# Kernel optimization log

Measured on AMD Instinct MI355X. Metric: run time of the kernel, lower is better.

## Reference

```python
import jax, jax.numpy as jnp
import numpy as np

FEAT_STRIDE = 16
PRE_NMS_TOP_N = 6000
POST_NMS_TOP_N = 300
NMS_THRESH = 0.7
A = 9  # len(scales)*len(ratios)
NEG = jnp.float32(-1e10)


def _generate_base_anchors(base_size=16, ratios=(0.5, 1.0, 2.0), scales=(8, 16, 32)):
    ratios = np.array(ratios, dtype=np.float64)
    scales = np.array(scales, dtype=np.float64)
    ctr = (base_size - 1) * 0.5
    size = float(base_size * base_size)
    ws = np.round(np.sqrt(size / ratios))
    hs = np.round(ws * ratios)
    out = []
    for w, h in zip(ws, hs):
        ws2 = w * scales
        hs2 = h * scales
        out.append(np.stack([ctr - 0.5 * (ws2 - 1), ctr - 0.5 * (hs2 - 1),
                             ctr + 0.5 * (ws2 - 1), ctr + 0.5 * (hs2 - 1)], axis=1))
    return np.concatenate(out, axis=0).astype(np.float32)  # [A,4]


def _all_anchors(H, W):
    base = _generate_base_anchors()
    sx = np.arange(W) * FEAT_STRIDE
    sy = np.arange(H) * FEAT_STRIDE
    sx, sy = np.meshgrid(sx, sy)  # [H,W] each, y-major ravel matches HW flatten
    shifts = np.stack([sx.ravel(), sy.ravel(), sx.ravel(), sy.ravel()], axis=1).astype(np.float32)
    return (shifts[:, None, :] + base[None, :, :]).reshape(-1, 4)  # [H*W*A,4]


def _nms_image(boxes, scores):
    # Greedy NMS on [N,4] boxes / [N] scores; emits top POST_NMS_TOP_N kept (padded with 0s).
    x1, y1, x2, y2 = boxes[:, 0], boxes[:, 1], boxes[:, 2], boxes[:, 3]
    areas = (x2 - x1 + 1.0) * (y2 - y1 + 1.0)

    def body(i, carry):
        live, ob, os_ = carry
        idx = jnp.argmax(live)
        s = live[idx]
        valid = s > NEG * 0.5
        b = boxes[idx]
        xx1 = jnp.maximum(b[0], x1)
        yy1 = jnp.maximum(b[1], y1)
        xx2 = jnp.minimum(b[2], x2)
        yy2 = jnp.minimum(b[3], y2)
        inter = jnp.maximum(xx2 - xx1 + 1.0, 0.0) * jnp.maximum(yy2 - yy1 + 1.0, 0.0)
        iou = inter / (areas[idx] + areas - inter)
        live = jnp.where(iou > NMS_THRESH, NEG, live)  # suppresses self too (iou=1)
        ob = ob.at[i].set(jnp.where(valid, b, 0.0))
        os_ = os_.at[i].set(jnp.where(valid, s, 0.0))
        return live, ob, os_

    init = (scores,
            jnp.zeros((POST_NMS_TOP_N, 4), boxes.dtype),
            jnp.zeros((POST_NMS_TOP_N,), scores.dtype))
    _, ob, os_ = jax.lax.fori_loop(0, POST_NMS_TOP_N, body, init)
    return ob, os_


def setup_inputs() -> dict:
    key = jax.random.key(0)
    ks = jax.random.split(key, 4)
    B, C, H, W = 4, 1024, 64, 64
    base_feat = jax.random.normal(ks[0], (B, C, H, W), jnp.float32)
    im_info = jnp.tile(jnp.array([H * 16.0, W * 16.0, 1.0], jnp.float32), (B, 1))
    gt_boxes = jnp.zeros((B, 20, 5), jnp.float32)   # unused in eval path
    num_boxes = jnp.zeros((B,), jnp.int32)           # unused in eval path
    conv_w = 0.01 * jax.random.normal(ks[1], (512, C, 3, 3), jnp.float32)
    conv_b = jnp.zeros((512,), jnp.float32)
    cls_w = 0.01 * jax.random.normal(ks[2], (2 * A, 512, 1, 1), jnp.float32)
    cls_b = jnp.zeros((2 * A,), jnp.float32)
    bbox_w = 0.01 * jax.random.normal(ks[3], (4 * A, 512, 1, 1), jnp.float32)
    bbox_b = jnp.zeros((4 * A,), jnp.float32)
    return {"base_feat": base_feat, "im_info": im_info, "gt_boxes": gt_boxes,
            "num_boxes": num_boxes, "conv_w": conv_w, "conv_b": conv_b,
            "cls_w": cls_w, "cls_b": cls_b, "bbox_w": bbox_w, "bbox_b": bbox_b}


def reference(base_feat, im_info, gt_boxes, num_boxes, conv_w, conv_b, cls_w, cls_b, bbox_w, bbox_b):
    B, _, H, W = base_feat.shape
    dn = ("NCHW", "OIHW", "NCHW")
    x = jax.lax.conv_general_dilated(base_feat, conv_w, (1, 1), [(1, 1), (1, 1)], dimension_numbers=dn)
    x = jax.nn.relu(x + conv_b[None, :, None, None])  # RPN_Conv + ReLU, [B,512,H,W]
    cls = jax.lax.conv_general_dilated(x, cls_w, (1, 1), "VALID", dimension_numbers=dn) + cls_b[None, :, None, None]
    bbox = jax.lax.conv_general_dilated(x, bbox_w, (1, 1), "VALID", dimension_numbers=dn) + bbox_b[None, :, None, None]

    # reshape(x,2) -> softmax over the 2-way axis: channel c pairs with c+A
    prob = jax.nn.softmax(cls.reshape(B, 2, A, H, W), axis=1)
    fg = prob[:, 1]                                   # [B,A,H,W] foreground probs
    scores = fg.transpose(0, 2, 3, 1).reshape(B, -1)  # [B, H*W*A]
    deltas = bbox.transpose(0, 2, 3, 1).reshape(B, -1, 4)

    anchors = jnp.asarray(_all_anchors(H, W))         # [H*W*A,4]
    wa = anchors[:, 2] - anchors[:, 0] + 1.0
    ha = anchors[:, 3] - anchors[:, 1] + 1.0
    cxa = anchors[:, 0] + 0.5 * (wa - 1.0)
    cya = anchors[:, 1] + 0.5 * (ha - 1.0)

    cx = deltas[..., 0] * wa + cxa
    cy = deltas[..., 1] * ha + cya
    pw = jnp.exp(deltas[..., 2]) * wa
    ph = jnp.exp(deltas[..., 3]) * ha
    x1 = cx - 0.5 * pw
    y1 = cy - 0.5 * ph
    x2 = cx + 0.5 * pw
    y2 = cy + 0.5 * ph

    imh = im_info[:, 0:1]
    imw = im_info[:, 1:2]
    x1 = jnp.clip(x1, 0.0, imw - 1.0)
    y1 = jnp.clip(y1, 0.0, imh - 1.0)
    x2 = jnp.clip(x2, 0.0, imw - 1.0)
    y2 = jnp.clip(y2, 0.0, imh - 1.0)
    boxes = jnp.stack([x1, y1, x2, y2], axis=-1)      # [B,N,4]

    s_top, idx = jax.lax.top_k(scores, PRE_NMS_TOP_N)
    b_top = jnp.take_along_axis(boxes, idx[:, :, None], axis=1)  # [B,6000,4]

    kept_boxes, kept_scores = jax.vmap(_nms_image)(b_top, s_top)  # [B,300,4],[B,300]
    bidx = jnp.broadcast_to(jnp.arange(B, dtype=kept_boxes.dtype).reshape(B, 1, 1),
                            (B, POST_NMS_TOP_N, 1))
    rois = jnp.concatenate([bidx, kept_boxes], axis=-1)  # [B,300,5]
    return rois, kept_scores
```

## Files before the change

kernel.cpp:

```cpp
#include <hip/hip_runtime.h>
#include <stdint.h>

#define HH_ 64
#define WW_ 64
#define NB 4
#define CIN 1024
#define CMID 512
#define NANCH (HH_*WW_*9)
#define PRE_N 6000
#define POST_N 300
#define CAND_PAD 6144
#define NEGV (-1.0e10f)
#define LO_SCL 2048.0f
#define LO_INV 4.8828125e-4f
#define MWORDS 192

typedef unsigned short u16;
typedef unsigned long long u64;
typedef __attribute__((ext_vector_type(8))) _Float16 f16x8;
typedef __attribute__((ext_vector_type(4))) float f32x4;

#define AS1 __attribute__((address_space(1)))
#define AS3 __attribute__((address_space(3)))

#define X_OFF   0
#define X_SZ    (NB*CMID*HH_*WW_)
#define SC_OFF  (X_OFF + X_SZ)
#define SC_SZ   (NB*NANCH)
#define BX_OFF  (SC_OFF + SC_SZ)
#define BX_SZ   (NB*NANCH*4)
#define CSC_OFF (BX_OFF + BX_SZ)
#define CSC_SZ  (NB*CAND_PAD)
#define CBX_OFF (CSC_OFF + CSC_SZ)
#define CBX_SZ  (NB*CAND_PAD*4)
#define CIX_OFF (CBX_OFF + CBX_SZ)
#define CIX_SZ  (NB*CAND_PAD)
#define WTH_OFF (CIX_OFF + CIX_SZ)
#define WTH_SZ  (9*512*1024/2)
#define WTL_OFF (WTH_OFF + WTH_SZ)
#define WTL_SZ  WTH_SZ
#define XH_OFF  (WTL_OFF + WTL_SZ)
#define XH_SZ   (NB*4096*1024/2)
#define XL_OFF  (XH_OFF + XH_SZ)
#define XL_SZ   XH_SZ
#define ZP_OFF  (XL_OFF + XL_SZ)
#define ZP_SZ   256

__device__ __forceinline__ void gl2lds16(const void* g, void* l) {
    __builtin_amdgcn_global_load_lds((const AS1 unsigned int*)g,
                                     (AS3 unsigned int*)l, 16, 0, 0);
}
union fh_u { _Float16 h; u16 u; };
__device__ __forceinline__ u16 f2h_hi(float x) {
    fh_u c; c.h = (_Float16)x; return c.u;
}
__device__ __forceinline__ u16 f2h_lo(float x, u16 hi) {
    fh_u c; c.u = hi;
    float hf = (float)c.h;
    fh_u d; d.h = (_Float16)((x - hf) * LO_SCL);
    return d.u;
}
__device__ __forceinline__ int cperm(int c) {
    int blk = c >> 5, w = c & 31;
    int pos = (w < 16) ? (((w >> 2) << 3) + (w & 3))
                       : ((((w - 16) >> 2) << 3) + 4 + (w & 3));
    return (blk << 5) + pos;
}
__device__ __forceinline__ unsigned fflip(unsigned u) {
    return (u & 0x80000000u) ? ~u : (u | 0x80000000u);
}

__global__ __launch_bounds__(256) void prep_wtk(
    const float* __restrict__ conv_w, u16* __restrict__ WTH,
    u16* __restrict__ WTL, float* __restrict__ ZP)
{
    int o = blockIdx.x * 256 + threadIdx.x;
    int ci = o & 1023, co = (o >> 10) & 511, r = o >> 19;
    float v = conv_w[((size_t)(co * 1024 + ci)) * 9 + r];
    u16 h  = f2h_hi(v);
    u16 lo = f2h_lo(v, h);
    size_t d = (((size_t)(r * 512 + co)) << 10) + cperm(ci);
    WTH[d] = h; WTL[d] = lo;
    if (o < 256) ZP[o] = 0.f;
}

__global__ __launch_bounds__(256) void prep_act(
    const float* __restrict__ in, u16* __restrict__ XH, u16* __restrict__ XL)
{
    __shared__ float T[64][65];
    const int blk = blockIdx.x;
    const int b   = blk >> 10;
    const int ci0 = ((blk >> 6) & 15) << 6;
    const int sp0 = (blk & 63) << 6;
    const int tid = threadIdx.x;
    const int tq  = tid >> 6;
    const int t64 = tid & 63;
#pragma unroll
    for (int w = 0; w < 16; w++) {
        int ci_l = w * 4 + tq;
        T[ci_l][t64] = in[(((size_t)(b * 1024 + ci0 + ci_l)) << 12) + sp0 + t64];
    }
    __syncthreads();
#pragma unroll
    for (int w = 0; w < 16; w++) {
        int sp_l = w * 4 + tq;
        float x = T[t64][sp_l];
        u16 h  = f2h_hi(x);
        u16 lo = f2h_lo(x, h);
        size_t d = (((size_t)((b << 12) + sp0 + sp_l)) << 10) + ci0 + cperm(t64);
        XH[d] = h; XL[d] = lo;
    }
}

__global__ __launch_bounds__(256, 2) void conv3_mfma(
    const u16* __restrict__ WTH, const u16* __restrict__ WTL,
    const u16* __restrict__ XH, const u16* __restrict__ XL,
    const u16* __restrict__ ZP, const float* __restrict__ bias,
    float* __restrict__ Xout)
{
    __shared__ u16 Ah_s[2][4096];
    __shared__ u16 Al_s[2][4096];
    __shared__ u16 Bh_s[2][4096];
    __shared__ u16 Bl_s[2][4096];

    const int tid = threadIdx.x;
    const int bn  = blockIdx.x;
    const int bm  = blockIdx.y;
    const int l   = tid & 63;
    const int wid = tid >> 6, wm = wid >> 1, wn = wid & 1;

    const int rowq = tid >> 2;
    const int c8   = (tid & 3) << 3;

    int spb[2]; unsigned vmq[2];
#pragma unroll
    for (int q = 0; q < 2; q++) {
        int n = bn * 128 + q * 64 + rowq;
        int yy = (n >> 6) & 63, xx = n & 63;
        spb[q] = n;
        unsigned m9 = 0;
#pragma unroll
        for (int rr = 0; rr < 9; rr++) {
            int dy = rr / 3 - 1, dx = rr % 3 - 1;
            if ((unsigned)(yy + dy) < 64u && (unsigned)(xx + dx) < 64u)
                m9 |= 1u << rr;
        }
        vmq[q] = m9;
    }

    f32x4 acc0[4][4], acc1[4][4];
#pragma unroll
    for (int i = 0; i < 4; i++)
#pragma unroll
        for (int j = 0; j < 4; j++) { acc0[i][j] = (f32x4)0.f; acc1[i][j] = (f32x4)0.f; }

    const int NK = 288;

    auto stage = [&](int sb, int kt) {
        const int r   = kt >> 5;
        const int ci0 = (kt & 31) << 5;
        const int kr  = (r * 11) >> 5;
        const int sh  = (kr - 1) * 64 + (r - 3 * kr - 1);
        const size_t wbase = (((size_t)(r * 512 + bm * 128)) << 10) + ci0 + c8;
        u16* ah = &Ah_s[sb][tid * 8];
        u16* al = &Al_s[sb][tid * 8];
        u16* bh = &Bh_s[sb][tid * 8];
        u16* bl = &Bl_s[sb][tid * 8];
#pragma unroll
        for (int q = 0; q < 2; q++) {
            const size_t aoff = wbase + (((size_t)(q * 64 + rowq)) << 10);
            gl2lds16(WTH + aoff, ah + q * 2048);
            gl2lds16(WTL + aoff, al + q * 2048);
            const bool v = (vmq[q] >> r) & 1u;
            const size_t boff = (((size_t)(spb[q] + sh)) << 10) + ci0 + c8;
            gl2lds16(v ? (XH + boff) : ZP, bh + q * 2048);
            gl2lds16(v ? (XL + boff) : ZP, bl + q * 2048);
        }
    };

    stage(0, 0);
    int buf = 0;
    for (int kt = 0; kt < NK; ++kt) {
        __syncthreads();
        if (kt + 1 < NK) stage(buf ^ 1, kt + 1);
        {
            const int lo16 = l & 15, hi4 = l >> 4;
            const int aoff = (wm * 64 + lo16) * 32 + hi4 * 8;
            const int boff = (wn * 64 + lo16) * 32 + hi4 * 8;
            f16x8 ah[4], av[4], bh[4], bv[4];
#pragma unroll
            for (int i = 0; i < 4; i++) {
                ah[i] = *(const f16x8*)&Ah_s[buf][aoff + i * 512];
                av[i] = *(const f16x8*)&Al_s[buf][aoff + i * 512];
                bh[i] = *(const f16x8*)&Bh_s[buf][boff + i * 512];
                bv[i] = *(const f16x8*)&Bl_s[buf][boff + i * 512];
            }
#pragma unroll
            for (int mi = 0; mi < 4; mi++)
#pragma unroll
                for (int ni = 0; ni < 4; ni++) {
                    acc0[mi][ni] = __builtin_amdgcn_mfma_f32_16x16x32_f16(
                        ah[mi], bh[ni], acc0[mi][ni], 0, 0, 0);
                    acc1[mi][ni] = __builtin_amdgcn_mfma_f32_16x16x32_f16(
                        ah[mi], bv[ni], acc1[mi][ni], 0, 0, 0);
                    acc1[mi][ni] = __builtin_amdgcn_mfma_f32_16x16x32_f16(
                        av[mi], bh[ni], acc1[mi][ni], 0, 0, 0);
                }
        }
        buf ^= 1;
    }

#pragma unroll
    for (int mi = 0; mi < 4; mi++) {
        const int co0 = bm * 128 + wm * 64 + mi * 16 + ((l >> 4) << 2);
        const f32x4 b4 = *(const f32x4*)&bias[co0];
#pragma unroll
        for (int ni = 0; ni < 4; ni++) {
            const int n = bn * 128 + wn * 64 + ni * 16 + (l & 15);
            const int b = n >> 12, sp = n & 4095;
            f32x4 v0 = acc0[mi][ni], v1 = acc1[mi][ni];
            float* xo = Xout + (((size_t)(b * 512 + co0)) << 12) + sp;
            xo[0]        = fmaxf(fmaf(v1[0], LO_INV, v0[0]) + b4[0], 0.f);
            xo[4096]     = fmaxf(fmaf(v1[1], LO_INV, v0[1]) + b4[1], 0.f);
            xo[2 * 4096] = fmaxf(fmaf(v1[2], LO_INV, v0[2]) + b4[2], 0.f);
            xo[3 * 4096] = fmaxf(fmaf(v1[3], LO_INV, v0[3]) + b4[3], 0.f);
        }
    }
}

__global__ __launch_bounds__(256) void heads_kernel(
    const float* __restrict__ X, const float* __restrict__ cls_w,
    const float* __restrict__ cls_b, const float* __restrict__ bbox_w,
    const float* __restrict__ bbox_b, const float* __restrict__ im_info,
    float* __restrict__ SC, float* __restrict__ BXo)
{
    __shared__ float Ws[54][64];
    const int tid = threadIdx.x;
    const int blk = blockIdx.x;
    const int b   = blk >> 4;
    const int s   = ((blk & 15) << 8) + tid;

    float acc[54];
#pragma unroll
    for (int j = 0; j < 18; j++) acc[j] = cls_b[j];
#pragma unroll
    for (int j = 0; j < 36; j++) acc[18 + j] = bbox_b[j];

    const float* xp = X + (size_t)b * CMID * 4096 + s;
    for (int c0 = 0; c0 < 512; c0 += 64) {
        __syncthreads();
        for (int e = tid; e < 54 * 64; e += 256) {
            int j = e >> 6, ci = e & 63;
            Ws[j][ci] = (j < 18) ? cls_w[j * 512 + c0 + ci]
                                 : bbox_w[(j - 18) * 512 + c0 + ci];
        }
        __syncthreads();
        for (int ci = 0; ci < 64; ci += 4) {
            float x0 = xp[(size_t)(c0 + ci) * 4096];
            float x1 = xp[(size_t)(c0 + ci + 1) * 4096];
            float x2 = xp[(size_t)(c0 + ci + 2) * 4096];
            float x3 = xp[(size_t)(c0 + ci + 3) * 4096];
#pragma unroll
            for (int j = 0; j < 54; j++) {
                float4 w4 = *(const float4*)&Ws[j][ci];
                acc[j] = fmaf(x3, w4.w, fmaf(x2, w4.z, fmaf(x1, w4.y, fmaf(x0, w4.x, acc[j]))));
            }
        }
    }

    const float imh = im_info[b * 3 + 0];
    const float imw = im_info[b * 3 + 1];
    const int hh = s >> 6, ww = s & 63;
    const float cxa = 7.5f + 16.f * (float)ww;
    const float cya = 7.5f + 16.f * (float)hh;
    const float WA[9] = {184.f, 368.f, 736.f, 128.f, 256.f, 512.f, 88.f, 176.f, 352.f};
    const float HA[9] = {96.f, 192.f, 384.f, 128.f, 256.f, 512.f, 176.f, 352.f, 704.f};
    const size_t base = (size_t)b * NANCH + (size_t)s * 9;
#pragma unroll
    for (int c = 0; c < 9; c++) {
        float bg = acc[c], fg = acc[9 + c];
        float m  = fmaxf(bg, fg);
        float e0 = expf(bg - m), e1 = expf(fg - m);
        float p  = e1 / (e0 + e1);
        float dx = acc[18 + 4 * c], dy = acc[19 + 4 * c];
        float dw = acc[20 + 4 * c], dh = acc[21 + 4 * c];
        float wa = WA[c], ha = HA[c];
        float cx = dx * wa + cxa;
        float cy = dy * ha + cya;
        float pw = expf(dw) * wa;
        float ph = expf(dh) * ha;
        float x1 = cx - 0.5f * pw, y1 = cy - 0.5f * ph;
        float x2 = cx + 0.5f * pw, y2 = cy + 0.5f * ph;
        x1 = fminf(fmaxf(x1, 0.f), imw - 1.f);
        y1 = fminf(fmaxf(y1, 0.f), imh - 1.f);
        x2 = fminf(fmaxf(x2, 0.f), imw - 1.f);
        y2 = fminf(fmaxf(y2, 0.f), imh - 1.f);
        SC[base + c] = p;
        *(float4*)&BXo[(base + c) * 4] = make_float4(x1, y1, x2, y2);
    }
}

__global__ __launch_bounds__(1024) void select_kernel(
    const float* __restrict__ SC,
    float* __restrict__ CSC, int* __restrict__ CIX)
{
    const int b = blockIdx.x, tid = threadIdx.x;
    const float* sc = SC + (size_t)b * NANCH;
    const unsigned* bits = (const unsigned*)sc;
    __shared__ int s_cnt;
    __shared__ int s_c1, s_c2;
    __shared__ int s_tie[8192];

    unsigned lo = 0u, hi = 0x3f800001u;
    while (hi - lo > 1u) {
        unsigned mid = lo + ((hi - lo) >> 1);
        if (tid == 0) s_cnt = 0;
        __syncthreads();
        int c = 0;
        for (int i = tid; i < NANCH; i += 1024) c += (bits[i] >= mid) ? 1 : 0;
#pragma unroll
        for (int off = 32; off; off >>= 1) c += __shfl_down(c, off);
        if ((tid & 63) == 0) atomicAdd(&s_cnt, c);
        __syncthreads();
        int total = s_cnt;
        __syncthreads();
        if (total >= PRE_N) lo = mid; else hi = mid;
    }
    const unsigned ustar = lo;

    if (tid == 0) s_cnt = 0;
    __syncthreads();
    {
        int c = 0;
        for (int i = tid; i < NANCH; i += 1024) c += (bits[i] > ustar) ? 1 : 0;
#pragma unroll
        for (int off = 32; off; off >>= 1) c += __shfl_down(c, off);
        if ((tid & 63) == 0) atomicAdd(&s_cnt, c);
    }
    __syncthreads();
    const int n1 = s_cnt;
    __syncthreads();

    if (tid == 0) { s_c1 = 0; s_c2 = 0; }
    __syncthreads();

    float*  csc  = CSC + (size_t)b * CAND_PAD;
    int*    cix  = CIX + (size_t)b * CAND_PAD;

    for (int i = tid; i < NANCH; i += 1024) {
        unsigned u = bits[i];
        if (u > ustar) {
            int p = atomicAdd(&s_c1, 1);
            csc[p] = sc[i]; cix[p] = i;
        } else if (u == ustar) {
            int p = atomicAdd(&s_c2, 1);
            if (p < 8192) s_tie[p] = i;
        }
    }
    __syncthreads();
    int m = s_c2; if (m > 8192) m = 8192;
    const int need = PRE_N - n1;
    for (int i = tid; i < 8192; i += 1024)
        if (i >= m) s_tie[i] = 0x7fffffff;
    __syncthreads();

    for (int k = 2; k <= 8192; k <<= 1) {
        for (int j = k >> 1; j > 0; j >>= 1) {
            for (int t = tid; t < 8192; t += 1024) {
                int ixj = t ^ j;
                if (ixj > t) {
                    int va = s_tie[t], vb = s_tie[ixj];
                    bool up = ((t & k) == 0);
                    if ((va > vb) == up) { s_tie[t] = vb; s_tie[ixj] = va; }
                }
            }
            __syncthreads();
        }
    }
    for (int t = tid; t < need; t += 1024) {
        int i = s_tie[t];
        int p = n1 + t;
        if (i >= 0 && i < NANCH) {
            csc[p] = sc[i]; cix[p] = i;
        } else {
            csc[p] = -2.0e10f; cix[p] = 0x7fffffff;
        }
    }
    for (int p = PRE_N + tid; p < CAND_PAD; p += 1024) {
        csc[p] = -2.0e10f;
        cix[p] = 0x7fffffff;
    }
}

__global__ __launch_bounds__(1024) void sort_kernel(
    float* __restrict__ CSC, float* __restrict__ CBX,
    int* __restrict__ CIX, const float* __restrict__ BX)
{
    const int b = blockIdx.x, tid = threadIdx.x;
    float* csc = CSC + (size_t)b * CAND_PAD;
    int*   cix = CIX + (size_t)b * CAND_PAD;
    float4* cbx4 = (float4*)CBX + (size_t)b * CAND_PAD;
    const float4* bx4 = (const float4*)BX + (size_t)b * NANCH;
    __shared__ u64 sk[8192];

    for (int i = tid; i < 8192; i += 1024) {
        u64 key = 0ull;
        if (i < CAND_PAD) {
            unsigned khi = fflip(__float_as_uint(csc[i]));
            unsigned klo = ~((unsigned)cix[i]);
            key = ((u64)khi << 32) | klo;
        }
        sk[i] = key;
    }
    __syncthreads();
    for (int k = 2; k <= 8192; k <<= 1) {
        for (int j = k >> 1; j > 0; j >>= 1) {
            for (int t = tid; t < 8192; t += 1024) {
                int ixj = t ^ j;
                if (ixj > t) {
                    u64 a = sk[t], c2 = sk[ixj];
                    bool up = ((t & k) == 0);
                    if ((a < c2) == up) { sk[t] = c2; sk[ixj] = a; }
                }
            }
            __syncthreads();
        }
    }
    for (int i = tid; i < CAND_PAD; i += 1024) {
        u64 key = sk[i];
        unsigned khi = (unsigned)(key >> 32), klo = (unsigned)key;
        unsigned su = (khi & 0x80000000u) ? (khi ^ 0x80000000u) : ~khi;
        float sc = __uint_as_float(su);
        int ci = (int)(~klo);
        csc[i] = sc; cix[i] = ci;
        float4 pb;
        if (sc > -5.0e9f && (unsigned)ci < (unsigned)NANCH) pb = bx4[ci];
        else pb = make_float4(-4e9f, -4e9f, -4e9f, -4e9f);
        cbx4[i] = pb;
    }
}

__global__ __launch_bounds__(256) void nms_mask(
    const float* __restrict__ CBX, unsigned* __restrict__ MASK)
{
    const int rg = blockIdx.x, b = blockIdx.y, tid = threadIdx.x;
    const float4* cbx = (const float4*)CBX + (size_t)b * CAND_PAD;
    unsigned* mrow = MASK + (size_t)b * CAND_PAD * MWORDS;

    __shared__ float4 rb[64];
    __shared__ float  rar[64];
    __shared__ float4 cb[1024];
    __shared__ float  car[1024];

    if (tid < 64) {
        float4 v = cbx[rg * 64 + tid];
        rb[tid] = v;
        rar[tid] = (v.z - v.x + 1.f) * (v.w - v.y + 1.f);
    }
    __syncthreads();
    const int rl = tid >> 2;
    const int wq = tid & 3;
    const float4 rv = rb[rl];
    const float  ra = rar[rl];
    const size_t rbase = (size_t)(rg * 64 + rl) * MWORDS;

    for (int jt = rg >> 4; jt < 6; jt++) {
        __syncthreads();
        for (int e = tid; e < 1024; e += 256) {
            float4 v = cbx[jt * 1024 + e];
            cb[e] = v;
            car[e] = (v.z - v.x + 1.f) * (v.w - v.y + 1.f);
        }
        __syncthreads();
#pragma unroll
        for (int k = 0; k < 8; k++) {
            const int wt = wq + 4 * k;
            unsigned bits = 0;
            for (int bit = 0; bit < 32; bit++) {
                const int j = wt * 32 + bit;
                float4 cv = cb[j];
                float xx1 = fmaxf(rv.x, cv.x);
                float yy1 = fmaxf(rv.y, cv.y);
                float xx2 = fminf(rv.z, cv.z);
                float yy2 = fminf(rv.w, cv.w);
                float iw = fmaxf(xx2 - xx1 + 1.f, 0.f);
                float ih = fmaxf(yy2 - yy1 + 1.f, 0.f);
                float inter = iw * ih;
                float iou = inter / (ra + car[j] - inter);
                if (iou > 0.7f) bits |= (1u << bit);
            }
            mrow[rbase + jt * 32 + wt] = bits;
        }
    }
}

__global__ __launch_bounds__(1024) void nms_scan(
    const float* __restrict__ CSC, const float* __restrict__ CBX,
    const unsigned* __restrict__ MASK, float* __restrict__ out)
{
    const int b = blockIdx.x, tid = threadIdx.x;
    const float*  csc = CSC + (size_t)b * CAND_PAD;
    const float4* cbx = (const float4*)CBX + (size_t)b * CAND_PAD;
    const unsigned* mk = MASK + (size_t)b * CAND_PAD * MWORDS;

    __shared__ unsigned s_rm[MWORDS];
    __shared__ unsigned s_klo, s_khi;
    __shared__ int s_cnt;

    float* rois = out + (size_t)b * 1500;
    float* oscr = out + 6000 + (size_t)b * 300;

    if (tid < MWORDS) s_rm[tid] = 0u;
    if (tid == 0) s_cnt = 0;
    for (int it = tid; it < POST_N; it += 1024) {
        float* r = rois + it * 5;
        r[0] = (float)b; r[1] = 0.f; r[2] = 0.f; r[3] = 0.f; r[4] = 0.f;
        oscr[it] = 0.f;
    }
    __syncthreads();

    const int lane = tid & 63, wv = tid >> 6;
    for (int c = 0; c < 94; c++) {
        int kc = s_cnt;
        if (kc >= POST_N) break;
        if (wv == 0) {
            const int i = c * 64 + lane;
            unsigned rlo = mk[(size_t)i * MWORDS + 2 * c];
            unsigned rhi = mk[(size_t)i * MWORDS + 2 * c + 1];
            unsigned gw = s_rm[2 * c + (lane >> 5)];
            bool alive = !((gw >> (lane & 31)) & 1u) && (csc[i] > -5.0e9f);
            u64 rem = __ballot(alive);
            u64 keptm = 0ull;
            while (rem) {
                int sl = __builtin_ctzll(rem);
                keptm |= 1ull << sl;
                unsigned blo = __shfl(rlo, sl);
                unsigned bhi = __shfl(rhi, sl);
                rem &= ~(((u64)bhi << 32) | (u64)blo);
                rem &= ~(1ull << sl);
            }
            if (lane == 0) { s_klo = (unsigned)keptm; s_khi = (unsigned)(keptm >> 32); }
        }
        __syncthreads();
        u64 keptm = ((u64)s_khi << 32) | (u64)s_klo;
        int base = kc;
        while (keptm && base < POST_N) {
            int sl = __builtin_ctzll(keptm);
            keptm &= keptm - 1ull;
            const int i = c * 64 + sl;
            if (tid < MWORDS) s_rm[tid] |= mk[(size_t)i * MWORDS + tid];
            if (tid == 0) {
                float4 pb = cbx[i];
                float* r = rois + base * 5;
                r[1] = pb.x; r[2] = pb.y; r[3] = pb.z; r[4] = pb.w;
                oscr[base] = csc[i];
            }
            base++;
        }
        if (tid == 0) s_cnt = base;
        __syncthreads();
    }
}

extern "C" void kernel_launch(void* const* d_in, const int* in_sizes, int n_in,
                              void* d_out, int out_size, void* d_ws, size_t ws_size,
                              hipStream_t stream)
{
    const float* base_feat = (const float*)d_in[0];
    const float* im_info   = (const float*)d_in[1];
    const float* conv_w    = (const float*)d_in[4];
    const float* conv_b    = (const float*)d_in[5];
    const float* cls_w     = (const float*)d_in[6];
    const float* cls_b     = (const float*)d_in[7];
    const float* bbox_w    = (const float*)d_in[8];
    const float* bbox_b    = (const float*)d_in[9];

    float* ws  = (float*)d_ws;
    float* X   = ws + X_OFF;
    float* SC  = ws + SC_OFF;
    float* BX  = ws + BX_OFF;
    float* CSC = ws + CSC_OFF;
    float* CBX = ws + CBX_OFF;
    int*   CIX = (int*)(ws + CIX_OFF);
    u16*   WTH = (u16*)(ws + WTH_OFF);
    u16*   WTL = (u16*)(ws + WTL_OFF);
    u16*   XHp = (u16*)(ws + XH_OFF);
    u16*   XLp = (u16*)(ws + XL_OFF);
    float* ZPf = ws + ZP_OFF;
    const u16* ZPu = (const u16*)ZPf;
    unsigned* MASK = (unsigned*)(ws + X_OFF);
    float* out = (float*)d_out;

    hipLaunchKernelGGL(prep_wtk, dim3(18432), dim3(256), 0, stream,
                       conv_w, WTH, WTL, ZPf);
    hipLaunchKernelGGL(prep_act, dim3(4096), dim3(256), 0, stream,
                       base_feat, XHp, XLp);
    hipLaunchKernelGGL(conv3_mfma, dim3(128, 4), dim3(256), 0, stream,
                       WTH, WTL, XHp, XLp, ZPu, conv_b, X);
    hipLaunchKernelGGL(heads_kernel, dim3(64), dim3(256), 0, stream,
                       X, cls_w, cls_b, bbox_w, bbox_b, im_info, SC, BX);
    hipLaunchKernelGGL(select_kernel, dim3(4), dim3(1024), 0, stream,
                       SC, CSC, CIX);
    hipLaunchKernelGGL(sort_kernel, dim3(4), dim3(1024), 0, stream,
                       CSC, CBX, CIX, BX);
    hipLaunchKernelGGL(nms_mask, dim3(96, 4), dim3(256), 0, stream,
                       CBX, MASK);
    hipLaunchKernelGGL(nms_scan, dim3(4), dim3(1024), 0, stream,
                       CSC, CBX, MASK, out);
}
```

Before: 1.385 ms.

## Replace threshold binary search with radix histogram select and single-wave NMS scan

The select kernel now finds the top-6000 score threshold with three histogram passes over the score bits (13+13+6 bits) instead of roughly thirty counting passes from a binary search. When there are few ties it ranks them directly rather than running a full 8192-element bitonic sort. The NMS scan runs as one 64-thread wave, which removes block-wide barriers, and it prefetches the next chunk's mask words and scores. The heads kernel stages 256 channels of weights per tile instead of 64, so it needs fewer barriers but uses more shared memory. The histogram passes rely on shared-memory atomics, which can contend on heavily populated bins.

New measurement: 1.254 ms. -9.5%, faster.

```diff
diff --git a/kernel.cpp b/kernel.cpp
--- a/kernel.cpp
+++ b/kernel.cpp
@@ -234,7 +234,7 @@
     const float* __restrict__ bbox_b, const float* __restrict__ im_info,
     float* __restrict__ SC, float* __restrict__ BXo)
 {
-    __shared__ float Ws[54][64];
+    __shared__ __attribute__((aligned(16))) float Ws[54][256];
     const int tid = threadIdx.x;
     const int blk = blockIdx.x;
     const int b   = blk >> 4;
@@ -247,15 +247,15 @@
     for (int j = 0; j < 36; j++) acc[18 + j] = bbox_b[j];
 
     const float* xp = X + (size_t)b * CMID * 4096 + s;
-    for (int c0 = 0; c0 < 512; c0 += 64) {
-        __syncthreads();
-        for (int e = tid; e < 54 * 64; e += 256) {
-            int j = e >> 6, ci = e & 63;
+    for (int c0 = 0; c0 < 512; c0 += 256) {
+        __syncthreads();
+        for (int e = tid; e < 54 * 256; e += 256) {
+            int j = e >> 8, ci = e & 255;
             Ws[j][ci] = (j < 18) ? cls_w[j * 512 + c0 + ci]
                                  : bbox_w[(j - 18) * 512 + c0 + ci];
         }
         __syncthreads();
-        for (int ci = 0; ci < 64; ci += 4) {
+        for (int ci = 0; ci < 256; ci += 4) {
             float x0 = xp[(size_t)(c0 + ci) * 4096];
             float x1 = xp[(size_t)(c0 + ci + 1) * 4096];
             float x2 = xp[(size_t)(c0 + ci + 2) * 4096];
@@ -305,47 +305,82 @@
     float* __restrict__ CSC, int* __restrict__ CIX)
 {
     const int b = blockIdx.x, tid = threadIdx.x;
+    const int lane = tid & 63, wv = tid >> 6;
     const float* sc = SC + (size_t)b * NANCH;
     const unsigned* bits = (const unsigned*)sc;
-    __shared__ int s_cnt;
+
+    __shared__ unsigned s_buf[8192];
+    __shared__ unsigned s_part[1024];
+    __shared__ unsigned s_wsum[16];
+    __shared__ unsigned s_sel[2];
     __shared__ int s_c1, s_c2;
-    __shared__ int s_tie[8192];
-
-    unsigned lo = 0u, hi = 0x3f800001u;
-    while (hi - lo > 1u) {
-        unsigned mid = lo + ((hi - lo) >> 1);
-        if (tid == 0) s_cnt = 0;
-        __syncthreads();
-        int c = 0;
-        for (int i = tid; i < NANCH; i += 1024) c += (bits[i] >= mid) ? 1 : 0;
-#pragma unroll
-        for (int off = 32; off; off >>= 1) c += __shfl_down(c, off);
-        if ((tid & 63) == 0) atomicAdd(&s_cnt, c);
-        __syncthreads();
-        int total = s_cnt;
-        __syncthreads();
-        if (total >= PRE_N) lo = mid; else hi = mid;
-    }
-    const unsigned ustar = lo;
-
-    if (tid == 0) s_cnt = 0;
-    __syncthreads();
-    {
-        int c = 0;
-        for (int i = tid; i < NANCH; i += 1024) c += (bits[i] > ustar) ? 1 : 0;
-#pragma unroll
-        for (int off = 32; off; off >>= 1) c += __shfl_down(c, off);
-        if ((tid & 63) == 0) atomicAdd(&s_cnt, c);
-    }
-    __syncthreads();
-    const int n1 = s_cnt;
-    __syncthreads();
+
+    auto findbin = [&](int nb, int bpt, unsigned target) -> uint2 {
+        unsigned mysum = 0;
+        const int base = tid * bpt;
+        if (base < nb)
+            for (int q = 0; q < bpt; q++) mysum += s_buf[base + q];
+        s_part[tid] = mysum;
+        unsigned wsum = mysum;
+#pragma unroll
+        for (int off = 32; off; off >>= 1) wsum += __shfl_down(wsum, off);
+        if (lane == 0) s_wsum[wv] = wsum;
+        __syncthreads();
+        unsigned cum = 0;
+        for (int w = wv + 1; w < 16; w++) cum += s_wsum[w];
+        for (int ll = lane + 1; ll < 64; ll++) cum += s_part[(wv << 6) + ll];
+        if (base < nb) {
+            unsigned c = cum;
+            for (int q = bpt - 1; q >= 0; q--) {
+                unsigned h = s_buf[base + q];
+                if (c < target && c + h >= target) { s_sel[0] = base + q; s_sel[1] = c; }
+                c += h;
+            }
+        }
+        __syncthreads();
+        uint2 r; r.x = s_sel[0]; r.y = s_sel[1];
+        __syncthreads();
+        return r;
+    };
+
+    for (int i = tid; i < 8192; i += 1024) s_buf[i] = 0;
+    __syncthreads();
+    for (int i = tid; i < NANCH; i += 1024)
+        atomicAdd(&s_buf[bits[i] >> 19], 1u);
+    __syncthreads();
+    uint2 r1 = findbin(8192, 8, PRE_N);
+    const unsigned B1 = r1.x;
+    unsigned target2 = PRE_N - r1.y;
+
+    for (int i = tid; i < 8192; i += 1024) s_buf[i] = 0;
+    __syncthreads();
+    for (int i = tid; i < NANCH; i += 1024) {
+        unsigned u = bits[i];
+        if ((u >> 19) == B1) atomicAdd(&s_buf[(u >> 6) & 8191u], 1u);
+    }
+    __syncthreads();
+    uint2 r2 = findbin(8192, 8, target2);
+    const unsigned B2 = r2.x;
+    unsigned target3 = target2 - r2.y;
+
+    for (int i = tid; i < 64; i += 1024) { }
+    if (tid < 64) s_buf[tid] = 0;
+    __syncthreads();
+    const unsigned pref26 = (B1 << 13) | B2;
+    for (int i = tid; i < NANCH; i += 1024) {
+        unsigned u = bits[i];
+        if ((u >> 6) == pref26) atomicAdd(&s_buf[u & 63u], 1u);
+    }
+    __syncthreads();
+    uint2 r3 = findbin(64, 1, target3);
+    const unsigned ustar = (B1 << 19) | (B2 << 6) | r3.x;
+    const int n1 = (int)(r1.y + r2.y + r3.y);
 
     if (tid == 0) { s_c1 = 0; s_c2 = 0; }
     __syncthreads();
-
-    float*  csc  = CSC + (size_t)b * CAND_PAD;
-    int*    cix  = CIX + (size_t)b * CAND_PAD;
+    float* csc = CSC + (size_t)b * CAND_PAD;
+    int*   cix = CIX + (size_t)b * CAND_PAD;
+    int* s_tie = (int*)s_buf;
 
     for (int i = tid; i < NANCH; i += 1024) {
         unsigned u = bits[i];
@@ -360,30 +395,39 @@
     __syncthreads();
     int m = s_c2; if (m > 8192) m = 8192;
     const int need = PRE_N - n1;
-    for (int i = tid; i < 8192; i += 1024)
-        if (i >= m) s_tie[i] = 0x7fffffff;
-    __syncthreads();
-
-    for (int k = 2; k <= 8192; k <<= 1) {
-        for (int j = k >> 1; j > 0; j >>= 1) {
-            for (int t = tid; t < 8192; t += 1024) {
-                int ixj = t ^ j;
-                if (ixj > t) {
-                    int va = s_tie[t], vb = s_tie[ixj];
-                    bool up = ((t & k) == 0);
-                    if ((va > vb) == up) { s_tie[t] = vb; s_tie[ixj] = va; }
+
+    if (m <= 1024) {
+        if (tid < m) {
+            int v = s_tie[tid];
+            int r = 0;
+            for (int j2 = 0; j2 < m; j2++) r += (s_tie[j2] < v) ? 1 : 0;
+            if (r < need) { csc[n1 + r] = sc[v]; cix[n1 + r] = v; }
+        }
+    } else {
+        for (int i = tid; i < 8192; i += 1024)
+            if (i >= m) s_tie[i] = 0x7fffffff;
+        __syncthreads();
+        for (int k = 2; k <= 8192; k <<= 1) {
+            for (int j = k >> 1; j > 0; j >>= 1) {
+                for (int t = tid; t < 8192; t += 1024) {
+                    int ixj = t ^ j;
+                    if (ixj > t) {
+                        int va = s_tie[t], vb = s_tie[ixj];
+                        bool up = ((t & k) == 0);
+                        if ((va > vb) == up) { s_tie[t] = vb; s_tie[ixj] = va; }
+                    }
                 }
-            }
-            __syncthreads();
-        }
-    }
-    for (int t = tid; t < need; t += 1024) {
-        int i = s_tie[t];
-        int p = n1 + t;
-        if (i >= 0 && i < NANCH) {
-            csc[p] = sc[i]; cix[p] = i;
-        } else {
-            csc[p] = -2.0e10f; cix[p] = 0x7fffffff;
+                __syncthreads();
+            }
+        }
+        for (int t = tid; t < need; t += 1024) {
+            int i = s_tie[t];
+            int p = n1 + t;
+            if (i >= 0 && i < NANCH) {
+                csc[p] = sc[i]; cix[p] = i;
+            } else {
+                csc[p] = -2.0e10f; cix[p] = 0x7fffffff;
+            }
         }
     }
     for (int p = PRE_N + tid; p < CAND_PAD; p += 1024) {
@@ -494,70 +538,68 @@
     }
 }
 
-__global__ __launch_bounds__(1024) void nms_scan(
+__global__ __launch_bounds__(64) void nms_scan(
     const float* __restrict__ CSC, const float* __restrict__ CBX,
     const unsigned* __restrict__ MASK, float* __restrict__ out)
 {
-    const int b = blockIdx.x, tid = threadIdx.x;
+    const int b = blockIdx.x, lane = threadIdx.x;
     const float*  csc = CSC + (size_t)b * CAND_PAD;
     const float4* cbx = (const float4*)CBX + (size_t)b * CAND_PAD;
     const unsigned* mk = MASK + (size_t)b * CAND_PAD * MWORDS;
 
     __shared__ unsigned s_rm[MWORDS];
-    __shared__ unsigned s_klo, s_khi;
-    __shared__ int s_cnt;
 
     float* rois = out + (size_t)b * 1500;
     float* oscr = out + 6000 + (size_t)b * 300;
 
-    if (tid < MWORDS) s_rm[tid] = 0u;
-    if (tid == 0) s_cnt = 0;
-    for (int it = tid; it < POST_N; it += 1024) {
+    for (int i = lane; i < MWORDS; i += 64) s_rm[i] = 0u;
+    for (int it = lane; it < POST_N; it += 64) {
         float* r = rois + it * 5;
         r[0] = (float)b; r[1] = 0.f; r[2] = 0.f; r[3] = 0.f; r[4] = 0.f;
         oscr[it] = 0.f;
     }
     __syncthreads();
 
-    const int lane = tid & 63, wv = tid >> 6;
-    for (int c = 0; c < 94; c++) {
-        int kc = s_cnt;
-        if (kc >= POST_N) break;
-        if (wv == 0) {
-            const int i = c * 64 + lane;
-            unsigned rlo = mk[(size_t)i * MWORDS + 2 * c];
-            unsigned rhi = mk[(size_t)i * MWORDS + 2 * c + 1];
-            unsigned gw = s_rm[2 * c + (lane >> 5)];
-            bool alive = !((gw >> (lane & 31)) & 1u) && (csc[i] > -5.0e9f);
-            u64 rem = __ballot(alive);
-            u64 keptm = 0ull;
-            while (rem) {
-                int sl = __builtin_ctzll(rem);
-                keptm |= 1ull << sl;
-                unsigned blo = __shfl(rlo, sl);
-                unsigned bhi = __shfl(rhi, sl);
-                rem &= ~(((u64)bhi << 32) | (u64)blo);
-                rem &= ~(1ull << sl);
-            }
-            if (lane == 0) { s_klo = (unsigned)keptm; s_khi = (unsigned)(keptm >> 32); }
-        }
-        __syncthreads();
-        u64 keptm = ((u64)s_khi << 32) | (u64)s_klo;
-        int base = kc;
-        while (keptm && base < POST_N) {
+    int cnt = 0;
+    unsigned rlo = mk[(size_t)lane * MWORDS + 0];
+    unsigned rhi = mk[(size_t)lane * MWORDS + 1];
+    float    rsc = csc[lane];
+
+    for (int c = 0; c < 94 && cnt < POST_N; c++) {
+        unsigned gw = s_rm[2 * c + (lane >> 5)];
+        bool alive = !((gw >> (lane & 31)) & 1u) && (rsc > -5.0e9f);
+        u64 rem = __ballot(alive);
+        u64 keptm = 0ull;
+        while (rem) {
+            int sl = __builtin_ctzll(rem);
+            keptm |= 1ull << sl;
+            unsigned blo = __shfl(rlo, sl);
+            unsigned bhi = __shfl(rhi, sl);
+            rem &= ~(((u64)bhi << 32) | (u64)blo);
+            rem &= ~(1ull << sl);
+        }
+        if (c + 1 < 94) {
+            const int i2 = (c + 1) * 64 + lane;
+            rlo = mk[(size_t)i2 * MWORDS + 2 * (c + 1)];
+            rhi = mk[(size_t)i2 * MWORDS + 2 * (c + 1) + 1];
+            rsc = csc[i2];
+        }
+        while (keptm && cnt < POST_N) {
             int sl = __builtin_ctzll(keptm);
             keptm &= keptm - 1ull;
             const int i = c * 64 + sl;
-            if (tid < MWORDS) s_rm[tid] |= mk[(size_t)i * MWORDS + tid];
-            if (tid == 0) {
+            const size_t rb = (size_t)i * MWORDS;
+            s_rm[lane]       |= mk[rb + lane];
+            s_rm[lane + 64]  |= mk[rb + lane + 64];
+            s_rm[lane + 128] |= mk[rb + lane + 128];
+            if (lane == 0) {
                 float4 pb = cbx[i];
-                float* r = rois + base * 5;
+                float* r = rois + cnt * 5;
                 r[1] = pb.x; r[2] = pb.y; r[3] = pb.z; r[4] = pb.w;
-                oscr[base] = csc[i];
-            }
-            base++;
-        }
-        if (tid == 0) s_cnt = base;
+                oscr[cnt] = csc[i];
+            }
+            cnt++;
+        }
         __syncthreads();
     }
 }
@@ -605,6 +647,6 @@
                        CSC, CBX, CIX, BX);
     hipLaunchKernelGGL(nms_mask, dim3(96, 4), dim3(256), 0, stream,
                        CBX, MASK);
-    hipLaunchKernelGGL(nms_scan, dim3(4), dim3(1024), 0, stream,
+    hipLaunchKernelGGL(nms_scan, dim3(4), dim3(64), 0, stream,
                        CSC, CBX, MASK, out);
 }
```
